# Kernel optimization log

Measured on AMD Instinct MI355X. Metric: run time of the kernel, lower is better.

## Reference

```python
import jax, jax.numpy as jnp
import numpy as np


def setup_inputs() -> dict:
    key = jax.random.key(0)
    ks = jax.random.split(key, 10)
    B, HD, CD = 8192, 1024, 1024
    stdv = 1.0 / np.sqrt(HD)
    inp = {
        "hprev": jax.random.normal(ks[0], (B, HD), dtype=jnp.float32),
        "cprev": jax.random.normal(ks[1], (B, CD), dtype=jnp.float32),
        "w_hi": jax.random.uniform(ks[2], (HD, CD), jnp.float32, -stdv, stdv),
        "b_hi": jax.random.uniform(ks[3], (1, CD), jnp.float32, -stdv, stdv),
        "w_hf": jax.random.uniform(ks[4], (HD, CD), jnp.float32, -stdv, stdv),
        "b_hf": jax.random.uniform(ks[5], (1, CD), jnp.float32, -stdv, stdv),
        "w_hg": jax.random.uniform(ks[6], (HD, CD), jnp.float32, -stdv, stdv),
        "b_hg": jax.random.uniform(ks[7], (1, CD), jnp.float32, -stdv, stdv),
        "w_ho": jax.random.uniform(ks[8], (HD, CD), jnp.float32, -stdv, stdv),
        "b_ho": jax.random.uniform(ks[9], (1, CD), jnp.float32, -stdv, stdv),
    }
    return inp


def reference(hprev, cprev, w_hi, b_hi, w_hf, b_hf, w_hg, b_hg, w_ho, b_ho):
    # LSTM cell gates driven only by previous hidden state.
    i = jax.nn.sigmoid(hprev @ w_hi + b_hi)   # input gate  [B, CD]
    f = jax.nn.sigmoid(hprev @ w_hf + b_hf)   # forget gate [B, CD]
    g = jnp.tanh(hprev @ w_hg + b_hg)         # cell candidate
    o = jax.nn.sigmoid(hprev @ w_ho + b_ho)   # output gate
    cprime = f * cprev + i * g
    hprime = o * jnp.tanh(cprime)
    return (hprime, cprime)
```

## Files before the change

kernel.cpp:

```cpp
#include <hip/hip_runtime.h>
#include <hip/hip_bf16.h>
#include <stdint.h>

typedef short short8 __attribute__((ext_vector_type(8)));
typedef float f32x4 __attribute__((ext_vector_type(4)));

#define MDIM 8192
#define KDIM 1024
#define NDIM 1024
#define NKT  16


__device__ __forceinline__ unsigned short f2bf(float f) {
  union { float f; unsigned int u; } v; v.f = f;
  unsigned int u = v.u;
  u += 0x7fffu + ((u >> 16) & 1u);
  return (unsigned short)(u >> 16);
}

__device__ __forceinline__ void load_lds16(const void* gsrc, void* ldst) {
  __builtin_amdgcn_global_load_lds(
      (__attribute__((address_space(1))) void*)gsrc,
      (__attribute__((address_space(3))) void*)ldst,
      16, 0, 0);
}

__device__ __forceinline__ float fast_sigmoid(float x) {
  return 1.0f / (1.0f + __expf(-x));
}

__device__ __forceinline__ float fast_tanh(float x) {
  x = fminf(30.0f, fmaxf(-30.0f, x));
  float e = __expf(-2.0f * x);
  return (1.0f - e) / (1.0f + e);
}


__global__ void convert_h_tiled(const float* __restrict__ in,
                                unsigned short* __restrict__ out, int nchunk) {
  int idx = blockIdx.x * blockDim.x + threadIdx.x;
  int stride = gridDim.x * blockDim.x;
  for (int i = idx; i < nchunk; i += stride) {
    int r = i >> 7;
    int kc8 = i & 127;
    const float4* src = reinterpret_cast<const float4*>(in + (size_t)r * KDIM + kc8 * 8);
    float4 v0 = src[0], v1 = src[1];
    short8 o;
    o[0] = (short)f2bf(v0.x); o[1] = (short)f2bf(v0.y);
    o[2] = (short)f2bf(v0.z); o[3] = (short)f2bf(v0.w);
    o[4] = (short)f2bf(v1.x); o[5] = (short)f2bf(v1.y);
    o[6] = (short)f2bf(v1.z); o[7] = (short)f2bf(v1.w);
    int kt = kc8 >> 3;
    int c8 = kc8 & 7;
    reinterpret_cast<short8*>(out)[((size_t)kt * MDIM + r) * 8 + c8] = o;
  }
}

__global__ void convert_w_tiled(const float* __restrict__ w0,
                                const float* __restrict__ w1,
                                const float* __restrict__ w2,
                                const float* __restrict__ w3,
                                unsigned short* __restrict__ out) {
  __shared__ float tile[64][65];
  int g = blockIdx.z;
  const float* w = (g == 0) ? w0 : (g == 1) ? w1 : (g == 2) ? w2 : w3;
  int kt = blockIdx.y;
  int k0 = kt * 64;
  int n0 = blockIdx.x * 64;
  int tx = threadIdx.x;
  int ty = threadIdx.y;
#pragma unroll
  for (int j = 0; j < 16; ++j) {
    int kk = ty * 16 + j;
    tile[kk][tx] = w[(size_t)(k0 + kk) * NDIM + n0 + tx];
  }
  __syncthreads();
#pragma unroll
  for (int j = 0; j < 16; ++j) {
    int nn = ty * 16 + j;
    out[(((size_t)kt * 4 + g) * NDIM + n0 + nn) * 64 + tx] = f2bf(tile[tx][nn]);
  }
}


#define X0 0
#define X1 65536

#define BAR() __builtin_amdgcn_s_barrier()
#define LGKM0() do { \
    asm volatile("s_waitcnt lgkmcnt(0)" ::: "memory"); \
    __builtin_amdgcn_sched_barrier(0); } while (0)
#define VM6() asm volatile("s_waitcnt vmcnt(6)" ::: "memory")

#define STG_A(BUF, ktv, h) do { \
    const uint32_t _oA = ((uint32_t)(ktv) << 20) + srcA + (h) * 16384; \
    load_lds16(ab + _oA,        ldsb + (BUF) + (h) * 16384 + tid * 16); \
    load_lds16(ab + _oA + 8192, ldsb + (BUF) + (h) * 16384 + 8192 + tid * 16); } while (0)
#define STG_B(BUF, ktv, h) do { \
    const uint32_t _oB = ((uint32_t)(ktv) << 19) + srcB0 + (h) * 262144; \
    load_lds16(bb + _oB,          ldsb + (BUF) + 32768 + (h) * 16384 + tid * 16); \
    load_lds16(bb + _oB + 131072, ldsb + (BUF) + 32768 + (h) * 16384 + 8192 + tid * 16); } while (0)

#define LDB_ALL(CB) do { \
    _Pragma("unroll") for (int g = 0; g < 4; ++g) { \
      Br[g * 2 + 0] = *(const short8*)(ldsb + (CB) + b_base + g * 8192 + s0v); \
      Br[g * 2 + 1] = *(const short8*)(ldsb + (CB) + b_base + g * 8192 + s1v); } } while (0)
#define LDA_Q(CB, qm) do { \
    _Pragma("unroll") for (int f = 0; f < 4; ++f) { \
      Ar[f * 2 + 0] = *(const short8*)(ldsb + (CB) + a_base + ((qm) * 64 + f * 16) * 128 + s0v); \
      Ar[f * 2 + 1] = *(const short8*)(ldsb + (CB) + a_base + ((qm) * 64 + f * 16) * 128 + s1v); } } while (0)

#define MFMAQ(qm, qn) do { \
    __builtin_amdgcn_s_setprio(1); \
    _Pragma("unroll") for (int kk = 0; kk < 2; ++kk) \
    _Pragma("unroll") for (int f = 0; f < 4; ++f) \
    _Pragma("unroll") for (int gg = 0; gg < 2; ++gg) \
      acc[(qn) * 2 + gg][(qm) * 4 + f] = __builtin_amdgcn_mfma_f32_16x16x32_bf16( \
          Ar[f * 2 + kk], Br[((qn) * 2 + gg) * 2 + kk], \
          acc[(qn) * 2 + gg][(qm) * 4 + f], 0, 0, 0); \
    __builtin_amdgcn_s_setprio(0); } while (0)

#define BLOCK4(CB, OB, tA1, tN2) do { \
     \
    LDB_ALL(CB); LDA_Q(CB, 0); \
    STG_A(OB, tA1, 1); \
    BAR(); LGKM0(); MFMAQ(0, 0); BAR(); \
     \
    STG_B(CB, tN2, 0); \
    BAR(); MFMAQ(0, 1); BAR(); \
     \
    LDA_Q(CB, 1); \
    STG_B(CB, tN2, 1); \
    BAR(); LGKM0(); MFMAQ(1, 0); BAR(); \
     \
    STG_A(CB, tN2, 0); \
    BAR(); MFMAQ(1, 1); VM6(); BAR(); } while (0)

__global__ __launch_bounds__(512, 2) void lstm_fused_gemm(
    const unsigned short* __restrict__ At,
    const unsigned short* __restrict__ Bt,
    const float* __restrict__ cprev,
    const float* __restrict__ b_i, const float* __restrict__ b_f,
    const float* __restrict__ b_g, const float* __restrict__ b_o,
    float* __restrict__ out)
{
  extern __shared__ unsigned char ldsb[];
  const int tid  = threadIdx.x;
  const int lane = tid & 63;
  const int wave = tid >> 6;
  const int wr = wave >> 2;
  const int wc = wave & 3;
  const int r15 = lane & 15;
  const int hh  = lane >> 4;

  int bid = blockIdx.x;
  int loc = bid >> 3;
  int nb = (bid & 7) * 2 + (loc >> 5);
  int mb = loc & 31;
  int brow = mb * 256;
  int bcol = nb * 64;

  const char* ab = (const char*)At;
  const char* bb = (const char*)Bt;

  const int srow = tid >> 3;
  const int cx = (((tid & 7) ^ (srow & 7)) << 4);
  const uint32_t srcA  = (uint32_t)(brow + srow) * 128 + cx;
  const uint32_t srcB0 = (uint32_t)(bcol + srow) * 128 + cx;

  const uint32_t a_base = (uint32_t)(wr * 128 + r15) * 128;
  const uint32_t b_base = 32768u + (uint32_t)(wc * 16 + r15) * 128;
  const int s0v = ((hh ^ (r15 & 7)) << 4);
  const int s1v = s0v ^ 64;

  f32x4 acc[4][8];
#pragma unroll
  for (int g = 0; g < 4; ++g)
#pragma unroll
    for (int m = 0; m < 8; ++m)
      acc[g][m] = (f32x4){0.f, 0.f, 0.f, 0.f};

  short8 Ar[8], Br[8];

  STG_A(X0, 0, 0); STG_A(X0, 0, 1);
  STG_B(X0, 0, 0); STG_B(X0, 0, 1);
  STG_B(X1, 1, 0); STG_B(X1, 1, 1);
  STG_A(X1, 1, 0);
  VM6();
  BAR();

  for (int it = 0; it < NKT / 2; ++it) {
    const int t0 = 2 * it;
    BLOCK4(X0, X1, (t0 + 1) & 15, (t0 + 2) & 15);
    BLOCK4(X1, X0, (t0 + 2) & 15, (t0 + 3) & 15);
  }

  const size_t outC = (size_t)MDIM * NDIM;
  const int cc = bcol + wc * 16 + r15;
  const float bi = b_i[cc], bff = b_f[cc], bg = b_g[cc], bo = b_o[cc];
#pragma unroll
  for (int m = 0; m < 8; ++m) {
#pragma unroll
    for (int j = 0; j < 4; ++j) {
      int rr = brow + wr * 128 + m * 16 + hh * 4 + j;
      size_t base = (size_t)rr * NDIM + cc;
      float pi = acc[0][m][j] + bi;
      float pf = acc[1][m][j] + bff;
      float pg = acc[2][m][j] + bg;
      float po = acc[3][m][j] + bo;
      float iv = fast_sigmoid(pi);
      float fv = fast_sigmoid(pf);
      float gv = fast_tanh(pg);
      float ov = fast_sigmoid(po);
      float cp = fv * cprev[base] + iv * gv;
      float hp = ov * fast_tanh(cp);
      out[base] = hp;
      out[outC + base] = cp;
    }
  }
}


extern "C" void kernel_launch(void* const* d_in, const int* in_sizes, int n_in,
                              void* d_out, int out_size, void* d_ws, size_t ws_size,
                              hipStream_t stream) {
  const float* hprev = (const float*)d_in[0];
  const float* cprev = (const float*)d_in[1];
  const float* w_hi  = (const float*)d_in[2];
  const float* b_hi  = (const float*)d_in[3];
  const float* w_hf  = (const float*)d_in[4];
  const float* b_hf  = (const float*)d_in[5];
  const float* w_hg  = (const float*)d_in[6];
  const float* b_hg  = (const float*)d_in[7];
  const float* w_ho  = (const float*)d_in[8];
  const float* b_ho  = (const float*)d_in[9];
  float* out = (float*)d_out;

  unsigned short* At = (unsigned short*)d_ws;
  unsigned short* Bt = (unsigned short*)((char*)d_ws + (size_t)NKT * MDIM * 64 * 2);

  convert_h_tiled<<<2048, 256, 0, stream>>>(hprev, At, MDIM * KDIM / 8);
  convert_w_tiled<<<dim3(16, 16, 4), dim3(64, 4, 1), 0, stream>>>(
      w_hi, w_hf, w_hg, w_ho, Bt);
  lstm_fused_gemm<<<512, 512, 131072, stream>>>(At, Bt, cprev,
                                                b_hi, b_hf, b_hg, b_ho, out);
}
```

Before: 105.6 us.

## Replace pipelined 256x64 GEMM with simple single-buffer 128x64 kernel using 32x32 MFMA

```diff
diff --git a/kernel.cpp b/kernel.cpp
--- a/kernel.cpp
+++ b/kernel.cpp
@@ -3,7 +3,7 @@
 #include <stdint.h>
 
 typedef short short8 __attribute__((ext_vector_type(8)));
-typedef float f32x4 __attribute__((ext_vector_type(4)));
+typedef float f32x16 __attribute__((ext_vector_type(16)));
 
 #define MDIM 8192
 #define KDIM 1024
@@ -83,60 +83,7 @@
 }
 
 
-#define X0 0
-#define X1 65536
-
-#define BAR() __builtin_amdgcn_s_barrier()
-#define LGKM0() do { \
-    asm volatile("s_waitcnt lgkmcnt(0)" ::: "memory"); \
-    __builtin_amdgcn_sched_barrier(0); } while (0)
-#define VM6() asm volatile("s_waitcnt vmcnt(6)" ::: "memory")
-
-#define STG_A(BUF, ktv, h) do { \
-    const uint32_t _oA = ((uint32_t)(ktv) << 20) + srcA + (h) * 16384; \
-    load_lds16(ab + _oA,        ldsb + (BUF) + (h) * 16384 + tid * 16); \
-    load_lds16(ab + _oA + 8192, ldsb + (BUF) + (h) * 16384 + 8192 + tid * 16); } while (0)
-#define STG_B(BUF, ktv, h) do { \
-    const uint32_t _oB = ((uint32_t)(ktv) << 19) + srcB0 + (h) * 262144; \
-    load_lds16(bb + _oB,          ldsb + (BUF) + 32768 + (h) * 16384 + tid * 16); \
-    load_lds16(bb + _oB + 131072, ldsb + (BUF) + 32768 + (h) * 16384 + 8192 + tid * 16); } while (0)
-
-#define LDB_ALL(CB) do { \
-    _Pragma("unroll") for (int g = 0; g < 4; ++g) { \
-      Br[g * 2 + 0] = *(const short8*)(ldsb + (CB) + b_base + g * 8192 + s0v); \
-      Br[g * 2 + 1] = *(const short8*)(ldsb + (CB) + b_base + g * 8192 + s1v); } } while (0)
-#define LDA_Q(CB, qm) do { \
-    _Pragma("unroll") for (int f = 0; f < 4; ++f) { \
-      Ar[f * 2 + 0] = *(const short8*)(ldsb + (CB) + a_base + ((qm) * 64 + f * 16) * 128 + s0v); \
-      Ar[f * 2 + 1] = *(const short8*)(ldsb + (CB) + a_base + ((qm) * 64 + f * 16) * 128 + s1v); } } while (0)
-
-#define MFMAQ(qm, qn) do { \
-    __builtin_amdgcn_s_setprio(1); \
-    _Pragma("unroll") for (int kk = 0; kk < 2; ++kk) \
-    _Pragma("unroll") for (int f = 0; f < 4; ++f) \
-    _Pragma("unroll") for (int gg = 0; gg < 2; ++gg) \
-      acc[(qn) * 2 + gg][(qm) * 4 + f] = __builtin_amdgcn_mfma_f32_16x16x32_bf16( \
-          Ar[f * 2 + kk], Br[((qn) * 2 + gg) * 2 + kk], \
-          acc[(qn) * 2 + gg][(qm) * 4 + f], 0, 0, 0); \
-    __builtin_amdgcn_s_setprio(0); } while (0)
-
-#define BLOCK4(CB, OB, tA1, tN2) do { \
-     \
-    LDB_ALL(CB); LDA_Q(CB, 0); \
-    STG_A(OB, tA1, 1); \
-    BAR(); LGKM0(); MFMAQ(0, 0); BAR(); \
-     \
-    STG_B(CB, tN2, 0); \
-    BAR(); MFMAQ(0, 1); BAR(); \
-     \
-    LDA_Q(CB, 1); \
-    STG_B(CB, tN2, 1); \
-    BAR(); LGKM0(); MFMAQ(1, 0); BAR(); \
-     \
-    STG_A(CB, tN2, 0); \
-    BAR(); MFMAQ(1, 1); VM6(); BAR(); } while (0)
-
-__global__ __launch_bounds__(512, 2) void lstm_fused_gemm(
+__global__ __launch_bounds__(256, 2) void lstm_fused_gemm(
     const unsigned short* __restrict__ At,
     const unsigned short* __restrict__ Bt,
     const float* __restrict__ cprev,
@@ -144,20 +91,20 @@
     const float* __restrict__ b_g, const float* __restrict__ b_o,
     float* __restrict__ out)
 {
-  extern __shared__ unsigned char ldsb[];
+  __shared__ unsigned char ldsb[49152];
   const int tid  = threadIdx.x;
   const int lane = tid & 63;
   const int wave = tid >> 6;
-  const int wr = wave >> 2;
-  const int wc = wave & 3;
-  const int r15 = lane & 15;
-  const int hh  = lane >> 4;
+  const int wr = wave >> 1;
+  const int wc = wave & 1;
+  const int l31 = lane & 31;
+  const int hb5 = lane >> 5;
 
   int bid = blockIdx.x;
-  int loc = bid >> 3;
-  int nb = (bid & 7) * 2 + (loc >> 5);
-  int mb = loc & 31;
-  int brow = mb * 256;
+  int swz = (bid & 7) * 128 + (bid >> 3);
+  int mb = swz >> 4;
+  int nb = swz & 15;
+  int brow = mb * 128;
   int bcol = nb * 64;
 
   const char* ab = (const char*)At;
@@ -165,49 +112,65 @@
 
   const int srow = tid >> 3;
   const int cx = (((tid & 7) ^ (srow & 7)) << 4);
-  const uint32_t srcA  = (uint32_t)(brow + srow) * 128 + cx;
-  const uint32_t srcB0 = (uint32_t)(bcol + srow) * 128 + cx;
-
-  const uint32_t a_base = (uint32_t)(wr * 128 + r15) * 128;
-  const uint32_t b_base = 32768u + (uint32_t)(wc * 16 + r15) * 128;
-  const int s0v = ((hh ^ (r15 & 7)) << 4);
-  const int s1v = s0v ^ 64;
-
-  f32x4 acc[4][8];
+  const uint32_t srcA = (uint32_t)(brow + srow) * 128 + cx;
+  const uint32_t srcB = (uint32_t)(bcol + srow) * 128 + cx;
+
+  int sx[4];
+#pragma unroll
+  for (int ks = 0; ks < 4; ++ks)
+    sx[ks] = (((ks * 2 + hb5) ^ (l31 & 7)) << 4);
+  const uint32_t a_row = (uint32_t)(wr * 64 + l31) * 128;
+  const uint32_t b_row = 16384u + (uint32_t)(wc * 32 + l31) * 128;
+
+  f32x16 acc[4][2];
 #pragma unroll
   for (int g = 0; g < 4; ++g)
 #pragma unroll
-    for (int m = 0; m < 8; ++m)
-      acc[g][m] = (f32x4){0.f, 0.f, 0.f, 0.f};
-
-  short8 Ar[8], Br[8];
-
-  STG_A(X0, 0, 0); STG_A(X0, 0, 1);
-  STG_B(X0, 0, 0); STG_B(X0, 0, 1);
-  STG_B(X1, 1, 0); STG_B(X1, 1, 1);
-  STG_A(X1, 1, 0);
-  VM6();
-  BAR();
-
-  for (int it = 0; it < NKT / 2; ++it) {
-    const int t0 = 2 * it;
-    BLOCK4(X0, X1, (t0 + 1) & 15, (t0 + 2) & 15);
-    BLOCK4(X1, X0, (t0 + 2) & 15, (t0 + 3) & 15);
+    for (int mf = 0; mf < 2; ++mf)
+#pragma unroll
+      for (int r = 0; r < 16; ++r)
+        acc[g][mf][r] = 0.f;
+
+  for (int t = 0; t < NKT; ++t) {
+#pragma unroll
+    for (int j = 0; j < 4; ++j)
+      load_lds16(ab + ((uint32_t)t << 20) + srcA + j * 4096,
+                 ldsb + j * 4096 + tid * 16);
+#pragma unroll
+    for (int g = 0; g < 4; ++g)
+#pragma unroll
+      for (int h = 0; h < 2; ++h)
+        load_lds16(bb + ((uint32_t)t << 19) + (uint32_t)g * 131072 + srcB + h * 4096,
+                   ldsb + 16384 + g * 8192 + h * 4096 + tid * 16);
+    __syncthreads();
+
+#pragma unroll
+    for (int ks = 0; ks < 4; ++ks) {
+      short8 A0 = *(const short8*)(ldsb + a_row + 0 * 4096 + sx[ks]);
+      short8 A1 = *(const short8*)(ldsb + a_row + 1 * 4096 + sx[ks]);
+#pragma unroll
+      for (int g = 0; g < 4; ++g) {
+        short8 Bg = *(const short8*)(ldsb + b_row + g * 8192 + sx[ks]);
+        acc[g][0] = __builtin_amdgcn_mfma_f32_32x32x16_bf16(A0, Bg, acc[g][0], 0, 0, 0);
+        acc[g][1] = __builtin_amdgcn_mfma_f32_32x32x16_bf16(A1, Bg, acc[g][1], 0, 0, 0);
+      }
+    }
+    __syncthreads();
   }
 
   const size_t outC = (size_t)MDIM * NDIM;
-  const int cc = bcol + wc * 16 + r15;
+  const int cc = bcol + wc * 32 + l31;
   const float bi = b_i[cc], bff = b_f[cc], bg = b_g[cc], bo = b_o[cc];
 #pragma unroll
-  for (int m = 0; m < 8; ++m) {
-#pragma unroll
-    for (int j = 0; j < 4; ++j) {
-      int rr = brow + wr * 128 + m * 16 + hh * 4 + j;
+  for (int mf = 0; mf < 2; ++mf) {
+#pragma unroll
+    for (int r = 0; r < 16; ++r) {
+      int rr = brow + wr * 64 + mf * 32 + (r & 3) + 8 * (r >> 2) + 4 * hb5;
       size_t base = (size_t)rr * NDIM + cc;
-      float pi = acc[0][m][j] + bi;
-      float pf = acc[1][m][j] + bff;
-      float pg = acc[2][m][j] + bg;
-      float po = acc[3][m][j] + bo;
+      float pi = acc[0][mf][r] + bi;
+      float pf = acc[1][mf][r] + bff;
+      float pg = acc[2][mf][r] + bg;
+      float po = acc[3][mf][r] + bo;
       float iv = fast_sigmoid(pi);
       float fv = fast_sigmoid(pf);
       float gv = fast_tanh(pg);
@@ -242,6 +205,6 @@
   convert_h_tiled<<<2048, 256, 0, stream>>>(hprev, At, MDIM * KDIM / 8);
   convert_w_tiled<<<dim3(16, 16, 4), dim3(64, 4, 1), 0, stream>>>(
       w_hi, w_hf, w_hg, w_ho, Bt);
-  lstm_fused_gemm<<<512, 512, 131072, stream>>>(At, Bt, cprev,
-                                                b_hi, b_hf, b_hg, b_ho, out);
-}
+  lstm_fused_gemm<<<1024, 256, 0, stream>>>(At, Bt, cprev,
+                                            b_hi, b_hf, b_hg, b_ho, out);
+}
```

New measurement: 115.0 us. 8.9% more time.
